# Optimization experiments

Measured on AMD Instinct MI355X. Metric: run time of the kernel, lower is better.

Reference implementation:

```python
import jax, jax.numpy as jnp
import numpy as np

VOCAB = 50265
D = 768
NUM_ROLES = 12
CODE_DEFAULT = 255 - 1  # fallback valid length for code
NL_DEFAULT = 127 - 1    # fallback valid length for nl


def _l2norm(x, eps=1e-12):
    n = jnp.sqrt(jnp.sum(x * x, axis=-1, keepdims=True))
    return x / jnp.maximum(n, eps)


def _valid_mask(ids, default_len):
    # first position where token == 2 (eos); if none, use default_len
    is2 = ids == 2
    has2 = jnp.any(is2, axis=1)
    first = jnp.argmax(is2, axis=1)
    total = jnp.where(has2, first, default_len)  # [B]
    S = ids.shape[1]
    return (jnp.arange(S)[None, :] < total[:, None]).astype(jnp.float32)


def setup_inputs() -> dict:
    key = jax.random.key(0)
    ks = jax.random.split(key, 12)
    B, Sc, Sn = 64, 640, 128
    code_inputs = jax.random.randint(ks[0], (B, Sc), 0, VOCAB)
    attn_mask = jax.random.randint(ks[1], (B, Sc, Sc), 0, 2).astype(bool)
    position_idx = jax.random.randint(ks[2], (B, Sc), 0, 5)
    nl_inputs = jax.random.randint(ks[3], (B, Sn), 0, VOCAB)
    role_indices = jax.random.randint(ks[4], (B, Sc), 0, NUM_ROLES)
    W_emb = jax.random.normal(ks[5], (VOCAB, D), dtype=jnp.float32) * 0.02
    role_table = jax.random.normal(ks[6], (NUM_ROLES, D), dtype=jnp.float32) * 0.02
    w_code = jax.random.normal(ks[7], (D,), dtype=jnp.float32) * 0.02
    b_code = jnp.zeros((), dtype=jnp.float32)
    w_nl = jax.random.normal(ks[8], (D,), dtype=jnp.float32) * 0.02
    b_nl = jnp.zeros((), dtype=jnp.float32)
    return {
        "code_inputs": code_inputs, "attn_mask": attn_mask,
        "position_idx": position_idx, "nl_inputs": nl_inputs,
        "role_indices": role_indices, "W_emb": W_emb,
        "role_table": role_table, "w_code": w_code, "b_code": b_code,
        "w_nl": w_nl, "b_nl": b_nl,
    }


def reference(code_inputs, attn_mask, position_idx, nl_inputs, role_indices,
              W_emb, role_table, w_code, b_code, w_nl, b_nl):
    # ---- code branch: DFG-node aggregation over code tokens ----
    nodes_mask = position_idx == 0            # [B,Sc] DFG nodes
    token_mask = position_idx >= 2            # [B,Sc] code tokens
    emb = W_emb[code_inputs]                  # [B,Sc,D]
    # dense node->token mask (the memory-bound tensor)
    m = (nodes_mask[:, :, None] & token_mask[:, None, :] & attn_mask).astype(emb.dtype)
    m = m / (jnp.sum(m, axis=-1, keepdims=True) + 1e-10)
    avg = jnp.einsum('bnt,btd->bnd', m, emb)  # masked-mean token embeddings per node
    mixed = jnp.where(nodes_mask[:, :, None], avg, emb)
    # encoder treated as identity (black-box HF encoder); custom math is faithful
    code_hidden = _l2norm(mixed)
    code_hwr = code_hidden + role_table[role_indices]
    code_probs = jax.nn.sigmoid(jnp.einsum('bsd,d->bs', code_hwr, w_code) + b_code)
    code_probs = code_probs * _valid_mask(code_inputs, CODE_DEFAULT)
    # ---- nl branch ----
    nl_hidden = _l2norm(W_emb[nl_inputs])
    nl_probs = jax.nn.sigmoid(jnp.einsum('bsd,d->bs', nl_hidden, w_nl) + b_nl)
    nl_probs = nl_probs * _valid_mask(nl_inputs, NL_DEFAULT)
    # ---- similarity matrix ----
    sim_mat = jnp.einsum('bnd,bmd->bnm', nl_hidden, code_hidden)  # [B,Sn,Sc]
    return (code_hidden, code_probs, nl_hidden, nl_probs, sim_mat)
```

## Files before the change

kernel.cpp:

```cpp
#include <hip/hip_runtime.h>

#define BB 64
#define SC 640
#define SN 128
#define DD 768
#define CODE_DEF 254
#define NL_DEF 126

typedef short bf16x8 __attribute__((ext_vector_type(8)));
typedef float f32x4 __attribute__((ext_vector_type(4)));

__device__ __forceinline__ unsigned short f2bf(float f) {
  unsigned u = __float_as_uint(f);
  u += 0x7fffu + ((u >> 16) & 1u);
  return (unsigned short)(u >> 16);
}

__global__ __launch_bounds__(64) void k0_prep(
    const int* __restrict__ code_ids, const int* __restrict__ nl_ids,
    const int* __restrict__ pos, const unsigned* __restrict__ attn_u32,
    int* __restrict__ nn, int* __restrict__ node_idx,
    int* __restrict__ len_code, int* __restrict__ len_nl,
    int* __restrict__ flag) {
  int b = blockIdx.x;
  int lane = threadIdx.x;
  int first = CODE_DEF;
  for (int c = 0; c < SC; c += 64) {
    bool is2 = code_ids[b * SC + c + lane] == 2;
    unsigned long long m = __ballot(is2);
    if (m) { first = c + __builtin_ctzll(m); break; }
  }
  int firstn = NL_DEF;
  for (int c = 0; c < SN; c += 64) {
    bool is2 = nl_ids[b * SN + c + lane] == 2;
    unsigned long long m = __ballot(is2);
    if (m) { firstn = c + __builtin_ctzll(m); break; }
  }
  int base = 0;
  for (int c = 0; c < SC; c += 64) {
    bool isn = pos[b * SC + c + lane] == 0;
    unsigned long long m = __ballot(isn);
    int pre = __popcll(m & ((1ull << lane) - 1ull));
    if (isn) node_idx[b * SC + base + pre] = c + lane;
    base += __popcll(m);
  }
  if (lane == 0) { nn[b] = base; len_code[b] = first; len_nl[b] = firstn; }
  if (b == 0) {
    int bad = 0;
    for (int i = lane; i < 1024; i += 64)
      if (attn_u32[i] > 1u) bad = 1;
    unsigned long long m = __ballot(bad);
    if (lane == 0) flag[0] = (m != 0ull) ? 1 : 0;
  }
}

__global__ __launch_bounds__(256) void k0b_mask(
    const int* __restrict__ attn, const int* __restrict__ pos,
    const int* __restrict__ nn, const int* __restrict__ node_idx,
    const int* __restrict__ flag,
    unsigned long long* __restrict__ mbits64, float* __restrict__ counts) {
  int id = blockIdx.x;
  int b = id & 63, g = id >> 6;
  int w = threadIdx.x >> 6, lane = threadIdx.x & 63;
  int count = nn[b];
  int isu8 = flag[0];
  for (int rr = 0; rr < 4; ++rr) {
    int slot = g * 16 + w * 4 + rr;
    long obase = ((long)b * 256 + slot) * 10;
    if (slot >= count) {
      if (lane < 10) mbits64[obase + lane] = 0ull;
      if (lane == 0) counts[b * 256 + slot] = 0.f;
      continue;
    }
    int nrow = node_idx[b * SC + slot];
    int tot = 0;
    for (int k = 0; k < 10; ++k) {
      int t = k * 64 + lane;
      bool tk = pos[b * SC + t] >= 2;
      bool av;
      if (isu8)
        av = ((const unsigned char*)attn)[((long)b * SC + nrow) * SC + t] != 0;
      else
        av = attn[((long)b * SC + nrow) * SC + t] != 0;
      unsigned long long m = __ballot(av && tk);
      if (lane == 0) mbits64[obase + k] = m;
      tot += __popcll(m);
    }
    if (lane == 0) counts[b * 256 + slot] = (float)tot;
  }
}

__global__ __launch_bounds__(256) void k2_mfma(
    const unsigned* __restrict__ mbits, const float* __restrict__ counts,
    const int* __restrict__ nn, const int* __restrict__ node_idx,
    const int* __restrict__ code_ids, const float* __restrict__ Wemb,
    float* __restrict__ codeh) {
  __shared__ unsigned short As[2][64 * 64];
  __shared__ unsigned short Bs[2][128 * 64];
  __shared__ int rowsidx[64];
  __shared__ int cid[SC];
  int id = blockIdx.x;
  int b = id & 63;
  int g = id >> 6;
  int nt = g & 3, dt = g >> 2;
  int count = nn[b];
  if (nt * 64 >= count) return;
  int tid = threadIdx.x;
  for (int i = tid; i < SC; i += 256) cid[i] = code_ids[b * SC + i];
  if (tid < 64) {
    int slot = nt * 64 + tid;
    rowsidx[tid] = (slot < count) ? node_idx[b * SC + slot] : -1;
  }
  __syncthreads();
  const int lane = tid & 63, w = tid >> 6, wm = w >> 1, wn = w & 1;
  const int dcol = dt * 128;

  f32x4 acc[2][4];
#pragma unroll
  for (int m = 0; m < 2; ++m)
#pragma unroll
    for (int n = 0; n < 4; ++n) acc[m][n] = (f32x4){0.f, 0.f, 0.f, 0.f};

  const int r_a = tid >> 2, q_ = tid & 3;
  const unsigned* mrow = mbits + ((long)b * 256 + nt * 64 + r_a) * 20;
  int tg4[2], d0[2];
#pragma unroll
  for (int q = 0; q < 2; ++q) {
    int task = tid + 256 * q;
    tg4[q] = task >> 5;
    d0[q] = (task & 31) * 4;
  }

  f32x4 va[2][4];
  unsigned bits16;

#define LOADC(cc)                                                          \
  {                                                                        \
    bits16 = (mrow[(cc) * 2 + (q_ >> 1)] >> ((q_ & 1) * 16)) & 0xffffu;    \
    _Pragma("unroll") for (int q = 0; q < 2; ++q)                          \
        _Pragma("unroll") for (int j = 0; j < 4; ++j) va[q][j] =           \
        *(const f32x4*)(Wemb +                                             \
                        (long)cid[(cc) * 64 + tg4[q] * 4 + j] * DD +       \
                        dcol + d0[q]);                                     \
  }

#define WRITEB(bf_)                                                        \
  {                                                                        \
    unsigned short* Ab = As[bf_];                                          \
    unsigned short* Bb = Bs[bf_];                                          \
    int tl = q_ * 16, sw = (r_a & 7) << 3;                                 \
    bf16x8 u0, u1;                                                         \
    _Pragma("unroll") for (int j = 0; j < 8; ++j) {                        \
      u0[j] = ((bits16 >> j) & 1u) ? (short)0x3F80 : (short)0;             \
      u1[j] = ((bits16 >> (8 + j)) & 1u) ? (short)0x3F80 : (short)0;       \
    }                                                                      \
    *(bf16x8*)(&Ab[r_a * 64 + (tl ^ sw)]) = u0;                            \
    *(bf16x8*)(&Ab[r_a * 64 + ((tl + 8) ^ sw)]) = u1;                      \
    _Pragma("unroll") for (int q = 0; q < 2; ++q)                          \
        _Pragma("unroll") for (int dj = 0; dj < 4; ++dj) {                 \
      int d = d0[q] + dj;                                                  \
      ushort4 u = {f2bf(va[q][0][dj]), f2bf(va[q][1][dj]),                 \
                   f2bf(va[q][2][dj]), f2bf(va[q][3][dj])};                \
      int s = ((((d >> 2) & 7) ^ ((d & 3) << 1)) << 3);                    \
      *(ushort4*)(&Bb[d * 64 + ((tg4[q] * 4) ^ s)]) = u;                   \
    }                                                                      \
  }

#define MFMAP(bf_)                                                         \
  {                                                                        \
    const unsigned short* Ab = As[bf_];                                    \
    const unsigned short* Bb = Bs[bf_];                                    \
    _Pragma("unroll") for (int ks = 0; ks < 2; ++ks) {                     \
      int kb = ks * 32 + (lane >> 4) * 8;                                  \
      bf16x8 af[2], bfv[4];                                                \
      _Pragma("unroll") for (int m = 0; m < 2; ++m) {                      \
        int rr = wm * 32 + m * 16 + (lane & 15);                           \
        af[m] = *(const bf16x8*)(&Ab[rr * 64 + (kb ^ ((rr & 7) << 3))]);   \
      }                                                                    \
      _Pragma("unroll") for (int n = 0; n < 4; ++n) {                      \
        int cc = wn * 64 + n * 16 + (lane & 15);                           \
        int s = ((((cc >> 2) & 7) ^ ((cc & 3) << 1)) << 3);                \
        bfv[n] = *(const bf16x8*)(&Bb[cc * 64 + (kb ^ s)]);                \
      }                                                                    \
      _Pragma("unroll") for (int m = 0; m < 2; ++m)                        \
          _Pragma("unroll") for (int n = 0; n < 4; ++n) acc[m][n] =        \
          __builtin_amdgcn_mfma_f32_16x16x32_bf16(af[m], bfv[n],           \
                                                  acc[m][n], 0, 0, 0);     \
    }                                                                      \
  }

  LOADC(0);
  WRITEB(0);
  __syncthreads();
  for (int c = 0; c < 10; ++c) {
    if (c < 9) LOADC(c + 1);
    MFMAP(c & 1);
    if (c < 9) WRITEB((c + 1) & 1);
    __syncthreads();
  }

  float* outb = codeh + (long)b * SC * DD + dcol + wn * 64;
#pragma unroll
  for (int m = 0; m < 2; ++m) {
    int row0 = wm * 32 + m * 16 + ((lane >> 4) << 2);
#pragma unroll
    for (int rr2 = 0; rr2 < 4; ++rr2) {
      int slotr = row0 + rr2;
      int nr = rowsidx[slotr];
      if (nr < 0) continue;
      float cnt = counts[b * 256 + nt * 64 + slotr];
      float inv = (cnt > 0.f) ? 1.f / cnt : 0.f;
      float* orow = outb + (long)nr * DD;
#pragma unroll
      for (int n = 0; n < 4; ++n)
        orow[n * 16 + (lane & 15)] = acc[m][n][rr2] * inv;
    }
  }
#undef LOADC
#undef WRITEB
#undef MFMAP
}

#define CODE_BLOCKS (BB * SC / 4)
__global__ __launch_bounds__(256) void k34_fused(
    const int* __restrict__ code_ids, const int* __restrict__ pos,
    const float* __restrict__ Wemb, float* __restrict__ codeh,
    const int* __restrict__ roles, const float* __restrict__ role_table,
    const float* __restrict__ w_code, const float* __restrict__ b_code,
    const int* __restrict__ len_code, float* __restrict__ code_probs,
    const int* __restrict__ nl_ids, const float* __restrict__ w_nl,
    const float* __restrict__ b_nl, const int* __restrict__ len_nl,
    float* __restrict__ nlh, float* __restrict__ nl_probs) {
  int w = threadIdx.x >> 6, lane = threadIdx.x & 63;
  if (blockIdx.x < CODE_BLOCKS) {
    long row = (long)blockIdx.x * 4 + w;
    int b = (int)(row / SC), s = (int)(row % SC);
    float* rp = codeh + row * DD;
    const float* src = (pos[row] == 0) ? rp : (Wemb + (long)code_ids[row] * DD);
    f32x4 x[3];
#pragma unroll
    for (int j = 0; j < 3; ++j)
      x[j] = *(const f32x4*)(src + lane * 4 + j * 256);
    float ss = 0.f;
#pragma unroll
    for (int j = 0; j < 3; ++j)
#pragma unroll
      for (int e = 0; e < 4; ++e) ss += x[j][e] * x[j][e];
#pragma unroll
    for (int o = 32; o > 0; o >>= 1) ss += __shfl_xor(ss, o, 64);
    float inv = 1.f / fmaxf(sqrtf(ss), 1e-12f);
    const float* rt = role_table + (long)roles[row] * DD;
    float dot = 0.f;
#pragma unroll
    for (int j = 0; j < 3; ++j) {
      f32x4 r = *(const f32x4*)(rt + lane * 4 + j * 256);
      f32x4 wc = *(const f32x4*)(w_code + lane * 4 + j * 256);
      f32x4 y;
#pragma unroll
      for (int e = 0; e < 4; ++e) {
        y[e] = x[j][e] * inv;
        dot += (y[e] + r[e]) * wc[e];
      }
      *(f32x4*)(rp + lane * 4 + j * 256) = y;
    }
#pragma unroll
    for (int o = 32; o > 0; o >>= 1) dot += __shfl_xor(dot, o, 64);
    if (lane == 0) {
      float p = 1.f / (1.f + expf(-(dot + b_code[0])));
      code_probs[row] = (s < len_code[b]) ? p : 0.f;
    }
  } else {
    long row = (long)(blockIdx.x - CODE_BLOCKS) * 4 + w;
    int b = (int)(row / SN), s = (int)(row % SN);
    const float* src = Wemb + (long)nl_ids[row] * DD;
    f32x4 x[3];
#pragma unroll
    for (int j = 0; j < 3; ++j)
      x[j] = *(const f32x4*)(src + lane * 4 + j * 256);
    float ss = 0.f;
#pragma unroll
    for (int j = 0; j < 3; ++j)
#pragma unroll
      for (int e = 0; e < 4; ++e) ss += x[j][e] * x[j][e];
#pragma unroll
    for (int o = 32; o > 0; o >>= 1) ss += __shfl_xor(ss, o, 64);
    float inv = 1.f / fmaxf(sqrtf(ss), 1e-12f);
    float* o = nlh + row * DD;
    float dot = 0.f;
#pragma unroll
    for (int j = 0; j < 3; ++j) {
      f32x4 wn = *(const f32x4*)(w_nl + lane * 4 + j * 256);
      f32x4 y;
#pragma unroll
      for (int e = 0; e < 4; ++e) {
        y[e] = x[j][e] * inv;
        dot += y[e] * wn[e];
      }
      *(f32x4*)(o + lane * 4 + j * 256) = y;
    }
#pragma unroll
    for (int of = 32; of > 0; of >>= 1) dot += __shfl_xor(dot, of, 64);
    if (lane == 0) {
      float p = 1.f / (1.f + expf(-(dot + b_nl[0])));
      nl_probs[row] = (s < len_nl[b]) ? p : 0.f;
    }
  }
}

__global__ __launch_bounds__(256) void k5_mfma(const float* __restrict__ nlh,
                                               const float* __restrict__ codeh,
                                               float* __restrict__ sim) {
  __shared__ unsigned short As[64 * 64];
  __shared__ unsigned short Bs[128 * 64];
  int id = blockIdx.x;
  int b = id & 63;
  int r = id >> 6;
  int nt = r % 2, ct = r / 2;
  int tid = threadIdx.x;
  int lane = tid & 63;
  int w = tid >> 6;
  int wm = w >> 1, wn = w & 1;

  f32x4 acc[2][4];
#pragma unroll
  for (int m = 0; m < 2; ++m)
#pragma unroll
    for (int n = 0; n < 4; ++n) acc[m][n] = (f32x4){0.f, 0.f, 0.f, 0.f};

  const float* Ag = nlh + ((long)b * SN + nt * 64) * DD;
  const float* Bg = codeh + ((long)b * SC + ct * 128) * DD;

  for (int c = 0; c < DD / 64; ++c) {
#pragma unroll
    for (int it = 0; it < 4; ++it) {
      int i = tid + 256 * it;
      int row = i >> 4, k0 = (i & 15) * 4;
      float4 va = *(const float4*)(Ag + (long)row * DD + c * 64 + k0);
      ushort4 ua = {f2bf(va.x), f2bf(va.y), f2bf(va.z), f2bf(va.w)};
      *(ushort4*)(&As[row * 64 + (k0 ^ ((row & 7) << 3))]) = ua;
    }
#pragma unroll
    for (int it = 0; it < 8; ++it) {
      int i = tid + 256 * it;
      int row = i >> 4, k0 = (i & 15) * 4;
      float4 vb = *(const float4*)(Bg + (long)row * DD + c * 64 + k0);
      ushort4 ub = {f2bf(vb.x), f2bf(vb.y), f2bf(vb.z), f2bf(vb.w)};
      *(ushort4*)(&Bs[row * 64 + (k0 ^ ((row & 7) << 3))]) = ub;
    }
    __syncthreads();
#pragma unroll
    for (int ks = 0; ks < 2; ++ks) {
      int kb = ks * 32 + (lane >> 4) * 8;
      bf16x8 af[2], bfr[4];
#pragma unroll
      for (int m = 0; m < 2; ++m) {
        int rr = wm * 32 + m * 16 + (lane & 15);
        af[m] = *(const bf16x8*)(&As[rr * 64 + (kb ^ ((rr & 7) << 3))]);
      }
#pragma unroll
      for (int n = 0; n < 4; ++n) {
        int rr = wn * 64 + n * 16 + (lane & 15);
        bfr[n] = *(const bf16x8*)(&Bs[rr * 64 + (kb ^ ((rr & 7) << 3))]);
      }
#pragma unroll
      for (int m = 0; m < 2; ++m)
#pragma unroll
        for (int n = 0; n < 4; ++n)
          acc[m][n] = __builtin_amdgcn_mfma_f32_16x16x32_bf16(
              af[m], bfr[n], acc[m][n], 0, 0, 0);
    }
    __syncthreads();
  }
  long ob = ((long)b * SN + nt * 64) * SC + ct * 128;
#pragma unroll
  for (int m = 0; m < 2; ++m) {
    int row0 = wm * 32 + m * 16 + ((lane >> 4) << 2);
#pragma unroll
    for (int n = 0; n < 4; ++n) {
      int col = wn * 64 + n * 16 + (lane & 15);
#pragma unroll
      for (int rr = 0; rr < 4; ++rr)
        sim[ob + (long)(row0 + rr) * SC + col] = acc[m][n][rr];
    }
  }
}

extern "C" void kernel_launch(void* const* d_in, const int* in_sizes, int n_in,
                              void* d_out, int out_size, void* d_ws,
                              size_t ws_size, hipStream_t stream) {
  const int* code_ids = (const int*)d_in[0];
  const int* attn = (const int*)d_in[1];
  const int* pos = (const int*)d_in[2];
  const int* nl_ids = (const int*)d_in[3];
  const int* roles = (const int*)d_in[4];
  const float* Wemb = (const float*)d_in[5];
  const float* role_table = (const float*)d_in[6];
  const float* w_code = (const float*)d_in[7];
  const float* b_code = (const float*)d_in[8];
  const float* w_nl = (const float*)d_in[9];
  const float* b_nl = (const float*)d_in[10];

  float* out = (float*)d_out;
  float* codeh = out;
  float* code_probs = out + 31457280;
  float* nlh = out + 31498240;
  float* nl_probs = out + 37789696;
  float* sim = out + 37797888;

  int* wsi = (int*)d_ws;
  int* nn = wsi;
  int* node_idx = wsi + 64;
  int* len_code = node_idx + BB * SC;
  int* len_nl = len_code + 64;
  int* flag = len_nl + 64;
  unsigned* mbits = (unsigned*)(wsi + 49152);
  float* counts = (float*)(wsi + 49152 + 327680);

  k0_prep<<<BB, 64, 0, stream>>>(code_ids, nl_ids, pos, (const unsigned*)attn,
                                 nn, node_idx, len_code, len_nl, flag);
  k0b_mask<<<BB * 16, 256, 0, stream>>>(attn, pos, nn, node_idx, flag,
                                        (unsigned long long*)mbits, counts);
  k2_mfma<<<BB * 24, 256, 0, stream>>>(mbits, counts, nn, node_idx, code_ids,
                                       Wemb, codeh);
  k34_fused<<<CODE_BLOCKS + BB * SN / 4, 256, 0, stream>>>(
      code_ids, pos, Wemb, codeh, roles, role_table, w_code, b_code, len_code,
      code_probs, nl_ids, w_nl, b_nl, len_nl, nlh, nl_probs);
  k5_mfma<<<BB * 10, 256, 0, stream>>>(nlh, codeh, sim);
}
```

Measured before the change: 170.5 us.

## Fuse node-token mask construction into the aggregation MFMA kernel

```diff
diff --git a/kernel.cpp b/kernel.cpp
--- a/kernel.cpp
+++ b/kernel.cpp
@@ -54,51 +54,17 @@
   }
 }
 
-__global__ __launch_bounds__(256) void k0b_mask(
+__global__ __launch_bounds__(256) void k2_mfma(
+    const int* __restrict__ nn, const int* __restrict__ node_idx,
+    const int* __restrict__ flag, const int* __restrict__ code_ids,
     const int* __restrict__ attn, const int* __restrict__ pos,
-    const int* __restrict__ nn, const int* __restrict__ node_idx,
-    const int* __restrict__ flag,
-    unsigned long long* __restrict__ mbits64, float* __restrict__ counts) {
-  int id = blockIdx.x;
-  int b = id & 63, g = id >> 6;
-  int w = threadIdx.x >> 6, lane = threadIdx.x & 63;
-  int count = nn[b];
-  int isu8 = flag[0];
-  for (int rr = 0; rr < 4; ++rr) {
-    int slot = g * 16 + w * 4 + rr;
-    long obase = ((long)b * 256 + slot) * 10;
-    if (slot >= count) {
-      if (lane < 10) mbits64[obase + lane] = 0ull;
-      if (lane == 0) counts[b * 256 + slot] = 0.f;
-      continue;
-    }
-    int nrow = node_idx[b * SC + slot];
-    int tot = 0;
-    for (int k = 0; k < 10; ++k) {
-      int t = k * 64 + lane;
-      bool tk = pos[b * SC + t] >= 2;
-      bool av;
-      if (isu8)
-        av = ((const unsigned char*)attn)[((long)b * SC + nrow) * SC + t] != 0;
-      else
-        av = attn[((long)b * SC + nrow) * SC + t] != 0;
-      unsigned long long m = __ballot(av && tk);
-      if (lane == 0) mbits64[obase + k] = m;
-      tot += __popcll(m);
-    }
-    if (lane == 0) counts[b * 256 + slot] = (float)tot;
-  }
-}
-
-__global__ __launch_bounds__(256) void k2_mfma(
-    const unsigned* __restrict__ mbits, const float* __restrict__ counts,
-    const int* __restrict__ nn, const int* __restrict__ node_idx,
-    const int* __restrict__ code_ids, const float* __restrict__ Wemb,
-    float* __restrict__ codeh) {
+    const float* __restrict__ Wemb, float* __restrict__ codeh) {
   __shared__ unsigned short As[2][64 * 64];
   __shared__ unsigned short Bs[2][128 * 64];
   __shared__ int rowsidx[64];
   __shared__ int cid[SC];
+  __shared__ unsigned long long tokm[10];
+  __shared__ float cnts_l[64];
   int id = blockIdx.x;
   int b = id & 63;
   int g = id >> 6;
@@ -106,14 +72,21 @@
   int count = nn[b];
   if (nt * 64 >= count) return;
   int tid = threadIdx.x;
+  const int lane = tid & 63, w = tid >> 6, wm = w >> 1, wn = w & 1;
   for (int i = tid; i < SC; i += 256) cid[i] = code_ids[b * SC + i];
   if (tid < 64) {
     int slot = nt * 64 + tid;
     rowsidx[tid] = (slot < count) ? node_idx[b * SC + slot] : -1;
   }
+  if (w == 0) {
+    for (int k = 0; k < 10; ++k) {
+      unsigned long long m = __ballot(pos[b * SC + k * 64 + lane] >= 2);
+      if (lane == 0) tokm[k] = m;
+    }
+  }
   __syncthreads();
-  const int lane = tid & 63, w = tid >> 6, wm = w >> 1, wn = w & 1;
   const int dcol = dt * 128;
+  const int isu8 = flag[0];
 
   f32x4 acc[2][4];
 #pragma unroll
@@ -122,7 +95,10 @@
     for (int n = 0; n < 4; ++n) acc[m][n] = (f32x4){0.f, 0.f, 0.f, 0.f};
 
   const int r_a = tid >> 2, q_ = tid & 3;
-  const unsigned* mrow = mbits + ((long)b * 256 + nt * 64 + r_a) * 20;
+  const int nrow_a = rowsidx[r_a];
+  const long arow = (nrow_a >= 0) ? ((long)b * SC + nrow_a) * SC : 0;
+  const unsigned char* attn_u8 = (const unsigned char*)attn;
+  int ptot = 0;
   int tg4[2], d0[2];
 #pragma unroll
   for (int q = 0; q < 2; ++q) {
@@ -136,7 +112,30 @@
 
 #define LOADC(cc)                                                          \
   {                                                                        \
-    bits16 = (mrow[(cc) * 2 + (q_ >> 1)] >> ((q_ & 1) * 16)) & 0xffffu;    \
+    unsigned tokq = (unsigned)((tokm[cc] >> (q_ * 16)) & 0xffffull);       \
+    unsigned ab = 0;                                                       \
+    if (nrow_a >= 0) {                                                     \
+      if (isu8) {                                                          \
+        uint4 v = *(const uint4*)(attn_u8 + arow + (cc) * 64 + q_ * 16);   \
+        _Pragma("unroll") for (int j = 0; j < 4; ++j) {                    \
+          ab |= (((v.x >> (8 * j)) & 0xffu) ? 1u : 0u) << j;               \
+          ab |= (((v.y >> (8 * j)) & 0xffu) ? 1u : 0u) << (4 + j);         \
+          ab |= (((v.z >> (8 * j)) & 0xffu) ? 1u : 0u) << (8 + j);         \
+          ab |= (((v.w >> (8 * j)) & 0xffu) ? 1u : 0u) << (12 + j);        \
+        }                                                                  \
+      } else {                                                             \
+        const int* ap = attn + arow + (cc) * 64 + q_ * 16;                 \
+        _Pragma("unroll") for (int j = 0; j < 4; ++j) {                    \
+          int4 v = *(const int4*)(ap + j * 4);                             \
+          ab |= (v.x ? 1u : 0u) << (4 * j);                                \
+          ab |= (v.y ? 1u : 0u) << (4 * j + 1);                            \
+          ab |= (v.z ? 1u : 0u) << (4 * j + 2);                            \
+          ab |= (v.w ? 1u : 0u) << (4 * j + 3);                            \
+        }                                                                  \
+      }                                                                    \
+    }                                                                      \
+    bits16 = ab & tokq;                                                    \
+    ptot += __popc(bits16);                                                \
     _Pragma("unroll") for (int q = 0; q < 2; ++q)                          \
         _Pragma("unroll") for (int j = 0; j < 4; ++j) va[q][j] =           \
         *(const f32x4*)(Wemb +                                             \
@@ -199,6 +198,13 @@
     __syncthreads();
   }
 
+  {
+    int t4 = ptot + __shfl_xor(ptot, 1, 64);
+    t4 += __shfl_xor(t4, 2, 64);
+    if (q_ == 0) cnts_l[r_a] = (float)t4;
+  }
+  __syncthreads();
+
   float* outb = codeh + (long)b * SC * DD + dcol + wn * 64;
 #pragma unroll
   for (int m = 0; m < 2; ++m) {
@@ -208,7 +214,7 @@
       int slotr = row0 + rr2;
       int nr = rowsidx[slotr];
       if (nr < 0) continue;
-      float cnt = counts[b * 256 + nt * 64 + slotr];
+      float cnt = cnts_l[slotr];
       float inv = (cnt > 0.f) ? 1.f / cnt : 0.f;
       float* orow = outb + (long)nr * DD;
 #pragma unroll
@@ -413,14 +419,10 @@
   int* len_code = node_idx + BB * SC;
   int* len_nl = len_code + 64;
   int* flag = len_nl + 64;
-  unsigned* mbits = (unsigned*)(wsi + 49152);
-  float* counts = (float*)(wsi + 49152 + 327680);
 
   k0_prep<<<BB, 64, 0, stream>>>(code_ids, nl_ids, pos, (const unsigned*)attn,
                                  nn, node_idx, len_code, len_nl, flag);
-  k0b_mask<<<BB * 16, 256, 0, stream>>>(attn, pos, nn, node_idx, flag,
-                                        (unsigned long long*)mbits, counts);
-  k2_mfma<<<BB * 24, 256, 0, stream>>>(mbits, counts, nn, node_idx, code_ids,
+  k2_mfma<<<BB * 24, 256, 0, stream>>>(nn, node_idx, flag, code_ids, attn, pos,
                                        Wemb, codeh);
   k34_fused<<<CODE_BLOCKS + BB * SN / 4, 256, 0, stream>>>(
       code_ids, pos, Wemb, codeh, roles, role_table, w_code, b_code, len_code,
```

Result: faster. 159.8 us (-6.3%).
